# Kernel tuning notes

Hardware: AMD Instinct MI355X
Metric: run time of the kernel (lower is better)

## Reference

```python
import jax, jax.numpy as jnp
import numpy as np

B, S, D_IN, H = 4, 2048, 1024, 1024


def setup_inputs() -> dict:
    key = jax.random.key(0)
    k1, k2, k3 = jax.random.split(key, 3)
    qkv = jax.random.normal(k1, (B, S, D_IN), dtype=jnp.float32)
    # True = position is masked out (torch masked_fill semantics)
    attention_mask = jax.random.randint(k2, (B, S), 0, 2).astype(jnp.bool_)
    W_qkv = jax.random.normal(k3, (D_IN, 3 * H), dtype=jnp.float32) * (1.0 / np.sqrt(D_IN))
    b_qkv = jnp.zeros((3 * H,), dtype=jnp.float32)
    return {"qkv": qkv, "attention_mask": attention_mask, "W_qkv": W_qkv, "b_qkv": b_qkv}


def reference(qkv, attention_mask, W_qkv, b_qkv):
    # fused QKV projection: (B, S, 3H)
    proj = jnp.einsum("bsd,dh->bsh", qkv, W_qkv) + b_qkv
    q, k, v = jnp.split(proj, 3, axis=-1)  # each (B, S, H)
    scaling_factor = jnp.asarray(H, dtype=q.dtype) ** 0.5
    q = q * scaling_factor  # NOTE: original multiplies (not divides) by sqrt(H)
    scores = jnp.einsum("bqh,bkh->bqk", q, k)  # (B, S, S)
    # mask broadcasts over the query dim: masked keys get -inf
    neg_inf = jnp.asarray(-jnp.inf, dtype=scores.dtype)
    scores = jnp.where(attention_mask[:, None, :], neg_inf, scores)
    distributions = jax.nn.softmax(scores, axis=-1)  # dropout p=0.0 -> identity
    return jnp.einsum("bqk,bkh->bqh", distributions, v)
```

## Files before the change

### kernel.cpp

```cpp
#include <hip/hip_runtime.h>
#include <stdint.h>


#define S_LEN 2048
#define BATCH 4
#define DIN   1024
#define HDIM  1024
#define N3H   3072
#define NTOK  8192

typedef unsigned short u16;
typedef __attribute__((ext_vector_type(8))) short bf16x8;
typedef __attribute__((ext_vector_type(4))) float f32x4;
typedef __attribute__((ext_vector_type(16))) float f32x16;
typedef __attribute__((ext_vector_type(4))) unsigned short u16x4;

__device__ __forceinline__ u16 f2bf(float x) {
  union { float f; unsigned u; } c; c.f = x;
  unsigned r = c.u + 0x7fffu + ((c.u >> 16) & 1u);
  return (u16)(r >> 16);
}
__device__ __forceinline__ float bf2f(u16 h) {
  union { unsigned u; float f; } c; c.u = ((unsigned)h) << 16;
  return c.f;
}

__device__ __forceinline__ void gload16(const void* g, void* lds) {
  auto* gp = reinterpret_cast<const __attribute__((address_space(1))) void*>(
      reinterpret_cast<uintptr_t>(g));
  auto* lp = reinterpret_cast<__attribute__((address_space(3))) void*>(
      (unsigned)reinterpret_cast<uintptr_t>(lds));
  __builtin_amdgcn_global_load_lds(gp, lp, 16, 0, 0);
}

__device__ __forceinline__ void stage_tile(const u16* __restrict__ g, int ld,
                                           u16* lds, int wave, int lane) {
  const int rlane = lane >> 3;
  const int kb    = (lane & 7) ^ (rlane & 7);
#pragma unroll
  for (int h = 0; h < 4; ++h) {
    const int instr = wave * 4 + h;
    const u16* gp = g + (size_t)(instr * 8 + rlane) * ld + kb * 8;
    gload16(gp, (char*)lds + instr * 1024);
  }
}

__device__ __forceinline__ bf16x8 frag32(const u16* t, int wq, int sub, int kh,
                                         int lane) {
  const int r5   = lane & 31;
  const int row  = wq * 64 + sub * 32 + r5;
  const int slot = (kh * 2 + (lane >> 5)) ^ (r5 & 7);
  return *(const bf16x8*)(t + row * 64 + slot * 8);
}

__device__ __forceinline__ void gemm_core_split(
    const u16* __restrict__ Ah, const u16* __restrict__ Al,
    const u16* __restrict__ Bh, const u16* __restrict__ Bl,
    int lda, int ldb, int K, f32x16 acc[2][2])
{
  __shared__ __align__(16) u16 lds[4 * 8192];
  u16* aH = lds;           u16* aL = lds + 8192;
  u16* bH = lds + 16384;   u16* bL = lds + 24576;
  const int tid  = threadIdx.x;
  const int wave = tid >> 6, lane = tid & 63;
  const int wm = wave >> 1, wn = wave & 1;

#pragma unroll
  for (int i = 0; i < 2; ++i)
#pragma unroll
    for (int j = 0; j < 2; ++j)
#pragma unroll
      for (int r = 0; r < 16; ++r) acc[i][j][r] = 0.f;

  for (int k0 = 0; k0 < K; k0 += 64) {
    stage_tile(Ah + k0, lda, aH, wave, lane);
    stage_tile(Al + k0, lda, aL, wave, lane);
    stage_tile(Bh + k0, ldb, bH, wave, lane);
    stage_tile(Bl + k0, ldb, bL, wave, lane);
    __syncthreads();

#pragma unroll
    for (int kh = 0; kh < 4; ++kh) {
      bf16x8 fah[2], fal[2];
#pragma unroll
      for (int i = 0; i < 2; ++i) {
        fah[i] = frag32(aH, wm, i, kh, lane);
        fal[i] = frag32(aL, wm, i, kh, lane);
      }
#pragma unroll
      for (int j = 0; j < 2; ++j) {
        const bf16x8 fbh = frag32(bH, wn, j, kh, lane);
        const bf16x8 fbl = frag32(bL, wn, j, kh, lane);
#pragma unroll
        for (int i = 0; i < 2; ++i) {
          acc[i][j] = __builtin_amdgcn_mfma_f32_32x32x16_bf16(fah[i], fbh, acc[i][j], 0, 0, 0);
          acc[i][j] = __builtin_amdgcn_mfma_f32_32x32x16_bf16(fah[i], fbl, acc[i][j], 0, 0, 0);
          acc[i][j] = __builtin_amdgcn_mfma_f32_32x32x16_bf16(fal[i], fbh, acc[i][j], 0, 0, 0);
        }
      }
    }
    __syncthreads();
  }
}

__device__ __forceinline__ void gemm_core_plain(
    const u16* __restrict__ A, const u16* __restrict__ B,
    int lda, int ldb, int K, f32x16 acc[2][2])
{
  __shared__ __align__(16) u16 lds[2 * 8192];
  u16* aT = lds; u16* bT = lds + 8192;
  const int tid  = threadIdx.x;
  const int wave = tid >> 6, lane = tid & 63;
  const int wm = wave >> 1, wn = wave & 1;

#pragma unroll
  for (int i = 0; i < 2; ++i)
#pragma unroll
    for (int j = 0; j < 2; ++j)
#pragma unroll
      for (int r = 0; r < 16; ++r) acc[i][j][r] = 0.f;

  for (int k0 = 0; k0 < K; k0 += 64) {
    stage_tile(A + k0, lda, aT, wave, lane);
    stage_tile(B + k0, ldb, bT, wave, lane);
    __syncthreads();
#pragma unroll
    for (int kh = 0; kh < 4; ++kh) {
      bf16x8 fa[2];
#pragma unroll
      for (int i = 0; i < 2; ++i) fa[i] = frag32(aT, wm, i, kh, lane);
#pragma unroll
      for (int j = 0; j < 2; ++j) {
        const bf16x8 fb = frag32(bT, wn, j, kh, lane);
#pragma unroll
        for (int i = 0; i < 2; ++i)
          acc[i][j] = __builtin_amdgcn_mfma_f32_32x32x16_bf16(fa[i], fb, acc[i][j], 0, 0, 0);
      }
    }
    __syncthreads();
  }
}

#define ROW32(r, lane) (((r) & 3) + 8 * ((r) >> 2) + 4 * ((lane) >> 5))

__global__ void prep_mask_kernel(const unsigned char* __restrict__ m,
                                 float* __restrict__ bias) {
  __shared__ int isBool;
  if (threadIdx.x == 0) isBool = 0;
  __syncthreads();
  for (int i = threadIdx.x; i < NTOK; i += 256)
    if ((i & 3) && m[i]) isBool = 1;
  __syncthreads();
  const int stride = isBool ? 1 : 4;
  const float ninf = -__builtin_inff();
  for (int i = threadIdx.x; i < NTOK; i += 256)
    bias[i] = m[(size_t)i * stride] ? ninf : 0.f;
}

__global__ __launch_bounds__(256) void split_f32_kernel(
    const float* __restrict__ x, u16* __restrict__ hi, u16* __restrict__ lo) {
  const int i = (blockIdx.x * 256 + threadIdx.x) * 4;
  const f32x4 v = *(const f32x4*)(x + i);
  u16x4 h, l;
#pragma unroll
  for (int c = 0; c < 4; ++c) {
    h[c] = f2bf(v[c]);
    l[c] = f2bf(v[c] - bf2f(h[c]));
  }
  *(u16x4*)(hi + i) = h;
  *(u16x4*)(lo + i) = l;
}

__global__ __launch_bounds__(256) void splitWT_kernel(
    const float* __restrict__ W, u16* __restrict__ whi, u16* __restrict__ wlo) {
  __shared__ float tile[32][33];
  const int t = threadIdx.x;
  const int n0 = blockIdx.x * 32;
  const int d0 = blockIdx.y * 32;
  const int dr = t >> 3, nc = (t & 7) * 4;
  const f32x4 v = *(const f32x4*)(W + (size_t)(d0 + dr) * N3H + n0 + nc);
#pragma unroll
  for (int c = 0; c < 4; ++c) tile[dr][nc + c] = v[c];
  __syncthreads();
  const int nr = t >> 3, dc = (t & 7) * 4;
  u16x4 h, l;
#pragma unroll
  for (int c = 0; c < 4; ++c) {
    const float x = tile[dc + c][nr];
    h[c] = f2bf(x);
    l[c] = f2bf(x - bf2f(h[c]));
  }
  const size_t o = (size_t)(n0 + nr) * DIN + d0 + dc;
  *(u16x4*)(whi + o) = h;
  *(u16x4*)(wlo + o) = l;
}

__global__ __launch_bounds__(256, 2) void proj_qk_kernel(
    const u16* __restrict__ Ahi, const u16* __restrict__ Alo,
    const u16* __restrict__ Whi, const u16* __restrict__ Wlo,
    const float* __restrict__ bias,
    u16* __restrict__ qhi, u16* __restrict__ qlo,
    u16* __restrict__ khi, u16* __restrict__ klo)
{
  const int bx = blockIdx.x, by = blockIdx.y;
  f32x16 acc[2][2];
  gemm_core_split(Ahi + (size_t)by * 128 * DIN, Alo + (size_t)by * 128 * DIN,
                  Whi + (size_t)bx * 128 * DIN, Wlo + (size_t)bx * 128 * DIN,
                  DIN, DIN, DIN, acc);
  const int lane = threadIdx.x & 63, wave = threadIdx.x >> 6;
  const int wm = wave >> 1, wn = wave & 1;
#pragma unroll
  for (int i = 0; i < 2; ++i) {
#pragma unroll
    for (int j = 0; j < 2; ++j) {
#pragma unroll
      for (int r = 0; r < 16; ++r) {
        const int row = by * 128 + wm * 64 + i * 32 + ROW32(r, lane);
        const int col = bx * 128 + wn * 64 + j * 32 + (lane & 31);
        const float v = acc[i][j][r] + bias[col];
        const u16 h = f2bf(v);
        const u16 l = f2bf(v - bf2f(h));
        if (col < HDIM) {
          const size_t idx = (size_t)row * HDIM + col;
          qhi[idx] = h; qlo[idx] = l;
        } else {
          const size_t idx = (size_t)row * HDIM + (col - HDIM);
          khi[idx] = h; klo[idx] = l;
        }
      }
    }
  }
}

__global__ __launch_bounds__(256, 2) void proj_v_kernel(
    const u16* __restrict__ Ahi, const u16* __restrict__ Whi,
    const float* __restrict__ bias, u16* __restrict__ vt)
{
  const int bx = blockIdx.x, by = blockIdx.y;
  f32x16 acc[2][2];
  gemm_core_plain(Ahi + (size_t)by * 128 * DIN,
                  Whi + (size_t)(2048 + bx * 128) * DIN,
                  DIN, DIN, DIN, acc);
  const int lane = threadIdx.x & 63, wave = threadIdx.x >> 6;
  const int wm = wave >> 1, wn = wave & 1;
#pragma unroll
  for (int i = 0; i < 2; ++i) {
#pragma unroll
    for (int j = 0; j < 2; ++j) {
#pragma unroll
      for (int r = 0; r < 16; ++r) {
        const int row = by * 128 + wm * 64 + i * 32 + ROW32(r, lane);
        const int b = row >> 11, s = row & 2047;
        const int hcol = bx * 128 + wn * 64 + j * 32 + (lane & 31);
        const float v = acc[i][j][r] + bias[2 * HDIM + hcol];
        vt[((size_t)b * HDIM + hcol) * S_LEN + s] = f2bf(v);
      }
    }
  }
}

__global__ __launch_bounds__(256, 2) void scores_kernel(
    const u16* __restrict__ qhi, const u16* __restrict__ qlo,
    const u16* __restrict__ khi, const u16* __restrict__ klo,
    const float* __restrict__ maskbias, float* __restrict__ scores)
{
  const int id   = blockIdx.x;
  const int xcd  = id & 7;
  const int s    = id >> 3;
  const int b    = s >> 5;
  const int slot = s & 31;
  const int r    = xcd + 8 * (slot >> 4);
  const int w    = slot & 15;
  const int bx   = (r & 3) * 4 + (w & 3);
  const int by   = (r >> 2) * 4 + (w >> 2);

  f32x16 acc[2][2];
  const size_t qoff = ((size_t)b * S_LEN + by * 128) * HDIM;
  const size_t koff = ((size_t)b * S_LEN + bx * 128) * HDIM;
  gemm_core_split(qhi + qoff, qlo + qoff, khi + koff, klo + koff,
                  HDIM, HDIM, HDIM, acc);
  const int lane = threadIdx.x & 63, wave = threadIdx.x >> 6;
  const int wm = wave >> 1, wn = wave & 1;
#pragma unroll
  for (int i = 0; i < 2; ++i) {
#pragma unroll
    for (int j = 0; j < 2; ++j) {
#pragma unroll
      for (int rr = 0; rr < 16; ++rr) {
        const int q   = by * 128 + wm * 64 + i * 32 + ROW32(rr, lane);
        const int key = bx * 128 + wn * 64 + j * 32 + (lane & 31);
        scores[((size_t)b * S_LEN + q) * S_LEN + key] =
            32.0f * acc[i][j][rr] + maskbias[b * S_LEN + key];
      }
    }
  }
}

__global__ __launch_bounds__(256) void softmax_kernel(float* __restrict__ scores) {
  const int wave = threadIdx.x >> 6, lane = threadIdx.x & 63;
  const int row = blockIdx.x * 4 + wave;
  float* srow = scores + (size_t)row * S_LEN;

  f32x4 v[8];
#pragma unroll
  for (int c = 0; c < 8; ++c) v[c] = ((const f32x4*)srow)[c * 64 + lane];

  float m = -__builtin_inff();
#pragma unroll
  for (int c = 0; c < 8; ++c)
    m = fmaxf(m, fmaxf(fmaxf(v[c][0], v[c][1]), fmaxf(v[c][2], v[c][3])));
#pragma unroll
  for (int o = 32; o > 0; o >>= 1) m = fmaxf(m, __shfl_xor(m, o));

  float s = 0.f;
#pragma unroll
  for (int c = 0; c < 8; ++c) {
#pragma unroll
    for (int e = 0; e < 4; ++e) {
      v[c][e] = __expf(v[c][e] - m);
      s += v[c][e];
    }
  }
#pragma unroll
  for (int o = 32; o > 0; o >>= 1) s += __shfl_xor(s, o);
  const float inv = 1.0f / s;

  u16* prow = (u16*)srow;
#pragma unroll
  for (int c = 0; c < 8; ++c) {
    u16x4 o4 = { f2bf(v[c][0] * inv), f2bf(v[c][1] * inv),
                 f2bf(v[c][2] * inv), f2bf(v[c][3] * inv) };
    ((u16x4*)prow)[c * 64 + lane] = o4;
  }
}

__global__ __launch_bounds__(256, 2) void pv_kernel(
    const u16* __restrict__ P, const u16* __restrict__ vt, float* __restrict__ out)
{
  const int id   = blockIdx.x;
  const int xcd  = id & 7;
  const int s    = id >> 3;
  const int b    = s >> 4;
  const int slot = s & 15;
  const int bx   = (xcd & 1) * 4 + (slot & 3);
  const int by   = (xcd >> 1) * 4 + (slot >> 2);

  f32x16 acc[2][2];
  gemm_core_plain(P + ((size_t)b * S_LEN + by * 128) * (2 * S_LEN),
                  vt + ((size_t)b * HDIM + bx * 128) * S_LEN,
                  2 * S_LEN, S_LEN, S_LEN, acc);
  const int lane = threadIdx.x & 63, wave = threadIdx.x >> 6;
  const int wm = wave >> 1, wn = wave & 1;
#pragma unroll
  for (int i = 0; i < 2; ++i) {
#pragma unroll
    for (int j = 0; j < 2; ++j) {
#pragma unroll
      for (int r = 0; r < 16; ++r) {
        const int q = by * 128 + wm * 64 + i * 32 + ROW32(r, lane);
        const int h = bx * 128 + wn * 64 + j * 32 + (lane & 31);
        out[((size_t)b * S_LEN + q) * HDIM + h] = acc[i][j][r];
      }
    }
  }
}

extern "C" void kernel_launch(void* const* d_in, const int* in_sizes, int n_in,
                              void* d_out, int out_size, void* d_ws, size_t ws_size,
                              hipStream_t stream)
{
  const float* qkv  = (const float*)d_in[0];
  const void*  mask = d_in[1];
  const float* W    = (const float*)d_in[2];
  const float* bias = (const float*)d_in[3];
  float* out = (float*)d_out;
  char* ws = (char*)d_ws;

  const size_t off_mask = 0;
  const size_t off_Whi  = 32768;
  const size_t off_Wlo  = off_Whi + (size_t)N3H * DIN * 2;
  const size_t off_Qhi  = off_Wlo + (size_t)N3H * DIN * 2;
  const size_t off_Qlo  = off_Qhi + (size_t)NTOK * HDIM * 2;
  const size_t off_Khi  = off_Qlo + (size_t)NTOK * HDIM * 2;
  const size_t off_Klo  = off_Khi + (size_t)NTOK * HDIM * 2;
  const size_t off_Vt   = off_Klo + (size_t)NTOK * HDIM * 2;
  const size_t off_A    = off_Vt + (size_t)NTOK * HDIM * 2;
  const size_t off_Alo  = off_A + (size_t)NTOK * DIN * 2;
  const size_t off_sc   = off_A;

  float* maskbias = (float*)(ws + off_mask);
  u16* Whi = (u16*)(ws + off_Whi);  u16* Wlo = (u16*)(ws + off_Wlo);
  u16* Qhi = (u16*)(ws + off_Qhi);  u16* Qlo = (u16*)(ws + off_Qlo);
  u16* Khi = (u16*)(ws + off_Khi);  u16* Klo = (u16*)(ws + off_Klo);
  u16* Vt  = (u16*)(ws + off_Vt);
  u16* Ahi = (u16*)(ws + off_A);    u16* Alo = (u16*)(ws + off_Alo);
  float* scores = (float*)(ws + off_sc);

  prep_mask_kernel<<<1, 256, 0, stream>>>((const unsigned char*)mask, maskbias);
  split_f32_kernel<<<NTOK * DIN / 1024, 256, 0, stream>>>(qkv, Ahi, Alo);
  splitWT_kernel<<<dim3(N3H / 32, DIN / 32), 256, 0, stream>>>(W, Whi, Wlo);
  proj_qk_kernel<<<dim3(2 * HDIM / 128, NTOK / 128, 1), 256, 0, stream>>>(
      Ahi, Alo, Whi, Wlo, bias, Qhi, Qlo, Khi, Klo);
  proj_v_kernel<<<dim3(HDIM / 128, NTOK / 128, 1), 256, 0, stream>>>(
      Ahi, Whi, bias, Vt);
  scores_kernel<<<16 * 16 * BATCH, 256, 0, stream>>>(
      Qhi, Qlo, Khi, Klo, maskbias, scores);
  softmax_kernel<<<NTOK / 4, 256, 0, stream>>>(scores);
  pv_kernel<<<8 * 16 * BATCH, 256, 0, stream>>>(
      (const u16*)scores, Vt, out);
}
```

Baseline: 414.5 us.

## Replace split-bf16 GEMM core with 256x256 double-buffered pipelined 8-wave kernel

The split-precision GEMM used by the QK projection and score kernels is rewritten. Each block now computes a 256x256 tile with 512 threads. The three hi/lo products are flattened into 48 K-steps over a double-buffered LDS, and the global-to-LDS loads for later steps are interleaved with MFMA phases using barriers, setprio and explicit vmcnt waits. This aims to hide global load latency and raise data reuse per byte loaded. In exchange it uses a large LDS footprint and has fewer blocks: the score kernel drops to 256 blocks and loses its XCD-aware block mapping.

Result: no change. 419.6 us (+1.2%).

```diff
diff --git a/kernel.cpp b/kernel.cpp
--- a/kernel.cpp
+++ b/kernel.cpp
@@ -45,6 +45,18 @@
   }
 }
 
+__device__ __forceinline__ void stage_half8(const u16* __restrict__ g, int ld,
+                                            u16* lds, int wave, int lane) {
+  const int rlane = lane >> 3;
+  const int kb    = (lane & 7) ^ (rlane & 7);
+#pragma unroll
+  for (int h = 0; h < 2; ++h) {
+    const int instr = wave * 2 + h;
+    const u16* gp = g + (size_t)(instr * 8 + rlane) * ld + kb * 8;
+    gload16(gp, (char*)lds + instr * 1024);
+  }
+}
+
 __device__ __forceinline__ bf16x8 frag32(const u16* t, int wq, int sub, int kh,
                                          int lane) {
   const int r5   = lane & 31;
@@ -53,54 +65,125 @@
   return *(const bf16x8*)(t + row * 64 + slot * 8);
 }
 
-__device__ __forceinline__ void gemm_core_split(
+__device__ __forceinline__ const u16* selA(const u16* Ah, const u16* Al, int t) {
+  return (t < 32) ? Ah : Al;
+}
+__device__ __forceinline__ const u16* selB(const u16* Bh, const u16* Bl, int t) {
+  return ((t >> 4) == 1) ? Bl : Bh;
+}
+
+template <int MODE>
+__device__ __forceinline__ void tile4(
+    int t, int buf, u16* lds, f32x16 acc[4][2],
     const u16* __restrict__ Ah, const u16* __restrict__ Al,
     const u16* __restrict__ Bh, const u16* __restrict__ Bl,
-    int lda, int ldb, int K, f32x16 acc[2][2])
-{
-  __shared__ __align__(16) u16 lds[4 * 8192];
-  u16* aH = lds;           u16* aL = lds + 8192;
-  u16* bH = lds + 16384;   u16* bL = lds + 24576;
-  const int tid  = threadIdx.x;
-  const int wave = tid >> 6, lane = tid & 63;
-  const int wm = wave >> 1, wn = wave & 1;
-
-#pragma unroll
-  for (int i = 0; i < 2; ++i)
-#pragma unroll
-    for (int j = 0; j < 2; ++j)
-#pragma unroll
-      for (int r = 0; r < 16; ++r) acc[i][j][r] = 0.f;
-
-  for (int k0 = 0; k0 < K; k0 += 64) {
-    stage_tile(Ah + k0, lda, aH, wave, lane);
-    stage_tile(Al + k0, lda, aL, wave, lane);
-    stage_tile(Bh + k0, ldb, bH, wave, lane);
-    stage_tile(Bl + k0, ldb, bL, wave, lane);
-    __syncthreads();
-
-#pragma unroll
-    for (int kh = 0; kh < 4; ++kh) {
-      bf16x8 fah[2], fal[2];
-#pragma unroll
-      for (int i = 0; i < 2; ++i) {
-        fah[i] = frag32(aH, wm, i, kh, lane);
-        fal[i] = frag32(aL, wm, i, kh, lane);
-      }
-#pragma unroll
-      for (int j = 0; j < 2; ++j) {
-        const bf16x8 fbh = frag32(bH, wn, j, kh, lane);
-        const bf16x8 fbl = frag32(bL, wn, j, kh, lane);
-#pragma unroll
-        for (int i = 0; i < 2; ++i) {
-          acc[i][j] = __builtin_amdgcn_mfma_f32_32x32x16_bf16(fah[i], fbh, acc[i][j], 0, 0, 0);
-          acc[i][j] = __builtin_amdgcn_mfma_f32_32x32x16_bf16(fah[i], fbl, acc[i][j], 0, 0, 0);
-          acc[i][j] = __builtin_amdgcn_mfma_f32_32x32x16_bf16(fal[i], fbh, acc[i][j], 0, 0, 0);
-        }
-      }
-    }
-    __syncthreads();
-  }
+    int lda, int ldb, int wm, int wn, int wave, int lane)
+{
+  u16* const Ab = lds + buf * 32768 + wm * 8192;
+  u16* const Bb = lds + buf * 32768 + 16384 + (wn >> 1) * 8192;
+  const int bs = wn & 1;
+  bf16x8 fa[2][4], fb0[4], fb1[4];
+
+#pragma unroll
+  for (int kh = 0; kh < 4; ++kh) {
+    fa[0][kh] = frag32(Ab, 0, 0, kh, lane);
+    fa[1][kh] = frag32(Ab, 0, 1, kh, lane);
+    fb0[kh]   = frag32(Bb, bs, 0, kh, lane);
+  }
+  if (MODE >= 1)
+    stage_half8(selA(Ah, Al, t + 1) + (size_t)128 * lda + ((t + 1) & 15) * 64,
+                lda, lds + ((t + 1) & 1) * 32768 + 8192, wave, lane);
+  __builtin_amdgcn_s_barrier();
+  __builtin_amdgcn_s_setprio(1);
+#pragma unroll
+  for (int kh = 0; kh < 4; ++kh) {
+    acc[0][0] = __builtin_amdgcn_mfma_f32_32x32x16_bf16(fa[0][kh], fb0[kh], acc[0][0], 0, 0, 0);
+    acc[1][0] = __builtin_amdgcn_mfma_f32_32x32x16_bf16(fa[1][kh], fb0[kh], acc[1][0], 0, 0, 0);
+  }
+  __builtin_amdgcn_s_setprio(0);
+  __builtin_amdgcn_s_barrier();
+
+#pragma unroll
+  for (int kh = 0; kh < 4; ++kh) fb1[kh] = frag32(Bb, bs, 1, kh, lane);
+  if (MODE >= 1)
+    stage_half8(selB(Bh, Bl, t + 1) + (size_t)128 * ldb + ((t + 1) & 15) * 64,
+                ldb, lds + ((t + 1) & 1) * 32768 + 24576, wave, lane);
+  __builtin_amdgcn_s_barrier();
+  __builtin_amdgcn_s_setprio(1);
+#pragma unroll
+  for (int kh = 0; kh < 4; ++kh) {
+    acc[0][1] = __builtin_amdgcn_mfma_f32_32x32x16_bf16(fa[0][kh], fb1[kh], acc[0][1], 0, 0, 0);
+    acc[1][1] = __builtin_amdgcn_mfma_f32_32x32x16_bf16(fa[1][kh], fb1[kh], acc[1][1], 0, 0, 0);
+  }
+  __builtin_amdgcn_s_setprio(0);
+  __builtin_amdgcn_s_barrier();
+  asm volatile("" ::: "memory");
+
+#pragma unroll
+  for (int kh = 0; kh < 4; ++kh) {
+    fa[0][kh] = frag32(Ab, 1, 0, kh, lane);
+    fa[1][kh] = frag32(Ab, 1, 1, kh, lane);
+  }
+  if (MODE == 2)
+    stage_half8(selB(Bh, Bl, t + 2) + ((t + 2) & 15) * 64, ldb,
+                lds + buf * 32768 + 16384, wave, lane);
+  __builtin_amdgcn_s_barrier();
+  __builtin_amdgcn_s_setprio(1);
+#pragma unroll
+  for (int kh = 0; kh < 4; ++kh) {
+    acc[2][0] = __builtin_amdgcn_mfma_f32_32x32x16_bf16(fa[0][kh], fb0[kh], acc[2][0], 0, 0, 0);
+    acc[3][0] = __builtin_amdgcn_mfma_f32_32x32x16_bf16(fa[1][kh], fb0[kh], acc[3][0], 0, 0, 0);
+  }
+  __builtin_amdgcn_s_setprio(0);
+  __builtin_amdgcn_s_barrier();
+  asm volatile("" ::: "memory");
+
+  if (MODE == 2) {
+    stage_half8(selA(Ah, Al, t + 2) + ((t + 2) & 15) * 64, lda,
+                lds + buf * 32768, wave, lane);
+    asm volatile("s_waitcnt vmcnt(4)" ::: "memory");
+  }
+  if (MODE == 1) asm volatile("s_waitcnt vmcnt(0)" ::: "memory");
+  __builtin_amdgcn_s_barrier();
+  __builtin_amdgcn_s_setprio(1);
+#pragma unroll
+  for (int kh = 0; kh < 4; ++kh) {
+    acc[2][1] = __builtin_amdgcn_mfma_f32_32x32x16_bf16(fa[0][kh], fb1[kh], acc[2][1], 0, 0, 0);
+    acc[3][1] = __builtin_amdgcn_mfma_f32_32x32x16_bf16(fa[1][kh], fb1[kh], acc[3][1], 0, 0, 0);
+  }
+  __builtin_amdgcn_s_setprio(0);
+  __builtin_amdgcn_s_barrier();
+}
+
+__device__ __forceinline__ void gemm256_split3(
+    const u16* __restrict__ Ah, const u16* __restrict__ Al,
+    const u16* __restrict__ Bh, const u16* __restrict__ Bl,
+    int lda, int ldb, f32x16 acc[4][2], u16* lds,
+    int wm, int wn, int wave, int lane)
+{
+#pragma unroll
+  for (int a = 0; a < 4; ++a)
+#pragma unroll
+    for (int b = 0; b < 2; ++b)
+#pragma unroll
+      for (int r = 0; r < 16; ++r) acc[a][b][r] = 0.f;
+
+  stage_half8(Ah, lda, lds, wave, lane);
+  stage_half8(Bh, ldb, lds + 16384, wave, lane);
+  stage_half8(Ah + (size_t)128 * lda, lda, lds + 8192, wave, lane);
+  stage_half8(Bh + (size_t)128 * ldb, ldb, lds + 24576, wave, lane);
+  stage_half8(Bh + 64, ldb, lds + 32768 + 16384, wave, lane);
+  stage_half8(Ah + 64, lda, lds + 32768, wave, lane);
+  asm volatile("s_waitcnt vmcnt(4)" ::: "memory");
+  __builtin_amdgcn_s_barrier();
+
+#pragma unroll 1
+  for (int t = 0; t < 46; t += 2) {
+    tile4<2>(t,     0, lds, acc, Ah, Al, Bh, Bl, lda, ldb, wm, wn, wave, lane);
+    tile4<2>(t + 1, 1, lds, acc, Ah, Al, Bh, Bl, lda, ldb, wm, wn, wave, lane);
+  }
+  tile4<1>(46, 0, lds, acc, Ah, Al, Bh, Bl, lda, ldb, wm, wn, wave, lane);
+  tile4<0>(47, 1, lds, acc, Ah, Al, Bh, Bl, lda, ldb, wm, wn, wave, lane);
 }
 
 __device__ __forceinline__ void gemm_core_plain(
@@ -195,29 +278,32 @@
   *(u16x4*)(wlo + o) = l;
 }
 
-__global__ __launch_bounds__(256, 2) void proj_qk_kernel(
+__global__ __launch_bounds__(512, 2) void proj_qk256_kernel(
     const u16* __restrict__ Ahi, const u16* __restrict__ Alo,
     const u16* __restrict__ Whi, const u16* __restrict__ Wlo,
     const float* __restrict__ bias,
     u16* __restrict__ qhi, u16* __restrict__ qlo,
     u16* __restrict__ khi, u16* __restrict__ klo)
 {
+  __shared__ __align__(16) u16 lds[2 * 4 * 8192];
   const int bx = blockIdx.x, by = blockIdx.y;
-  f32x16 acc[2][2];
-  gemm_core_split(Ahi + (size_t)by * 128 * DIN, Alo + (size_t)by * 128 * DIN,
-                  Whi + (size_t)bx * 128 * DIN, Wlo + (size_t)bx * 128 * DIN,
-                  DIN, DIN, DIN, acc);
-  const int lane = threadIdx.x & 63, wave = threadIdx.x >> 6;
-  const int wm = wave >> 1, wn = wave & 1;
-#pragma unroll
-  for (int i = 0; i < 2; ++i) {
-#pragma unroll
-    for (int j = 0; j < 2; ++j) {
+  const int tid = threadIdx.x, wave = tid >> 6, lane = tid & 63;
+  const int wm = wave >> 2, wn = wave & 3;
+
+  f32x16 acc[4][2];
+  gemm256_split3(Ahi + (size_t)by * 256 * DIN, Alo + (size_t)by * 256 * DIN,
+                 Whi + (size_t)bx * 256 * DIN, Wlo + (size_t)bx * 256 * DIN,
+                 DIN, DIN, acc, lds, wm, wn, wave, lane);
+
+#pragma unroll
+  for (int a = 0; a < 4; ++a) {
+#pragma unroll
+    for (int b = 0; b < 2; ++b) {
 #pragma unroll
       for (int r = 0; r < 16; ++r) {
-        const int row = by * 128 + wm * 64 + i * 32 + ROW32(r, lane);
-        const int col = bx * 128 + wn * 64 + j * 32 + (lane & 31);
-        const float v = acc[i][j][r] + bias[col];
+        const int row = by * 256 + wm * 128 + a * 32 + ROW32(r, lane);
+        const int col = bx * 256 + wn * 64 + b * 32 + (lane & 31);
+        const float v = acc[a][b][r] + bias[col];
         const u16 h = f2bf(v);
         const u16 l = f2bf(v - bf2f(h));
         if (col < HDIM) {
@@ -259,38 +345,35 @@
   }
 }
 
-__global__ __launch_bounds__(256, 2) void scores_kernel(
+__global__ __launch_bounds__(512, 2) void scores256_kernel(
     const u16* __restrict__ qhi, const u16* __restrict__ qlo,
     const u16* __restrict__ khi, const u16* __restrict__ klo,
     const float* __restrict__ maskbias, float* __restrict__ scores)
 {
-  const int id   = blockIdx.x;
-  const int xcd  = id & 7;
-  const int s    = id >> 3;
-  const int b    = s >> 5;
-  const int slot = s & 31;
-  const int r    = xcd + 8 * (slot >> 4);
-  const int w    = slot & 15;
-  const int bx   = (r & 3) * 4 + (w & 3);
-  const int by   = (r >> 2) * 4 + (w >> 2);
-
-  f32x16 acc[2][2];
-  const size_t qoff = ((size_t)b * S_LEN + by * 128) * HDIM;
-  const size_t koff = ((size_t)b * S_LEN + bx * 128) * HDIM;
-  gemm_core_split(qhi + qoff, qlo + qoff, khi + koff, klo + koff,
-                  HDIM, HDIM, HDIM, acc);
-  const int lane = threadIdx.x & 63, wave = threadIdx.x >> 6;
-  const int wm = wave >> 1, wn = wave & 1;
-#pragma unroll
-  for (int i = 0; i < 2; ++i) {
-#pragma unroll
-    for (int j = 0; j < 2; ++j) {
-#pragma unroll
-      for (int rr = 0; rr < 16; ++rr) {
-        const int q   = by * 128 + wm * 64 + i * 32 + ROW32(rr, lane);
-        const int key = bx * 128 + wn * 64 + j * 32 + (lane & 31);
+  __shared__ __align__(16) u16 lds[2 * 4 * 8192];
+  const int id = blockIdx.x;
+  const int b  = id >> 6;
+  const int by = (id >> 3) & 7;
+  const int bx = id & 7;
+  const int tid = threadIdx.x, wave = tid >> 6, lane = tid & 63;
+  const int wm = wave >> 2, wn = wave & 3;
+
+  f32x16 acc[4][2];
+  const size_t qoff = ((size_t)b * S_LEN + by * 256) * HDIM;
+  const size_t koff = ((size_t)b * S_LEN + bx * 256) * HDIM;
+  gemm256_split3(qhi + qoff, qlo + qoff, khi + koff, klo + koff,
+                 HDIM, HDIM, acc, lds, wm, wn, wave, lane);
+
+#pragma unroll
+  for (int a = 0; a < 4; ++a) {
+#pragma unroll
+    for (int bj = 0; bj < 2; ++bj) {
+#pragma unroll
+      for (int r = 0; r < 16; ++r) {
+        const int q   = by * 256 + wm * 128 + a * 32 + ROW32(r, lane);
+        const int key = bx * 256 + wn * 64 + bj * 32 + (lane & 31);
         scores[((size_t)b * S_LEN + q) * S_LEN + key] =
-            32.0f * acc[i][j][rr] + maskbias[b * S_LEN + key];
+            32.0f * acc[a][bj][r] + maskbias[b * S_LEN + key];
       }
     }
   }
@@ -399,11 +482,11 @@
   prep_mask_kernel<<<1, 256, 0, stream>>>((const unsigned char*)mask, maskbias);
   split_f32_kernel<<<NTOK * DIN / 1024, 256, 0, stream>>>(qkv, Ahi, Alo);
   splitWT_kernel<<<dim3(N3H / 32, DIN / 32), 256, 0, stream>>>(W, Whi, Wlo);
-  proj_qk_kernel<<<dim3(2 * HDIM / 128, NTOK / 128, 1), 256, 0, stream>>>(
+  proj_qk256_kernel<<<dim3(2 * HDIM / 256, NTOK / 256), 512, 0, stream>>>(
       Ahi, Alo, Whi, Wlo, bias, Qhi, Qlo, Khi, Klo);
   proj_v_kernel<<<dim3(HDIM / 128, NTOK / 128, 1), 256, 0, stream>>>(
       Ahi, Whi, bias, Vt);
-  scores_kernel<<<16 * 16 * BATCH, 256, 0, stream>>>(
+  scores256_kernel<<<64 * BATCH, 512, 0, stream>>>(
       Qhi, Qlo, Khi, Klo, maskbias, scores);
   softmax_kernel<<<NTOK / 4, 256, 0, stream>>>(scores);
   pv_kernel<<<8 * 16 * BATCH, 256, 0, stream>>>(
```

## Compact unmasked keys and skip masked key work across K/V projection and attention

Applied to the files above, without the earlier changes.

A prep kernel builds, per batch, a compacted list of unmasked key positions and their count. The K and V projections gather only those rows, and the scores, softmax and PV kernels then work only over the compacted key range, exiting early or shortening K beyond the count. With a random mask about half the keys are masked, so this removes roughly half of the K/V projection, score, softmax and PV work. In exchange it adds gather indirection in the tile loads and a serial single-block prep kernel, and the tail beyond the count relies on -inf padding inside softmax.

Result: faster. 382.2 us (-7.8%).

```diff
diff --git a/kernel.cpp b/kernel.cpp
--- a/kernel.cpp
+++ b/kernel.cpp
@@ -45,6 +45,20 @@
   }
 }
 
+__device__ __forceinline__ void stage_tile_idx(
+    const u16* __restrict__ gbase, const int* __restrict__ idxb, int jbase,
+    int k0, u16* lds, int wave, int lane) {
+  const int rlane = lane >> 3;
+  const int kb    = (lane & 7) ^ (rlane & 7);
+#pragma unroll
+  for (int h = 0; h < 4; ++h) {
+    const int instr = wave * 4 + h;
+    const int s = idxb[jbase + instr * 8 + rlane];
+    const u16* gp = gbase + (size_t)s * DIN + k0 + kb * 8;
+    gload16(gp, (char*)lds + instr * 1024);
+  }
+}
+
 __device__ __forceinline__ bf16x8 frag32(const u16* t, int wq, int sub, int kh,
                                          int lane) {
   const int r5   = lane & 31;
@@ -103,6 +117,57 @@
   }
 }
 
+__device__ __forceinline__ void gemm_core_split_idx(
+    const u16* __restrict__ Ah, const u16* __restrict__ Al,
+    const int* __restrict__ idxb, int jbase,
+    const u16* __restrict__ Bh, const u16* __restrict__ Bl,
+    f32x16 acc[2][2])
+{
+  __shared__ __align__(16) u16 lds[4 * 8192];
+  u16* aH = lds;           u16* aL = lds + 8192;
+  u16* bH = lds + 16384;   u16* bL = lds + 24576;
+  const int tid  = threadIdx.x;
+  const int wave = tid >> 6, lane = tid & 63;
+  const int wm = wave >> 1, wn = wave & 1;
+
+#pragma unroll
+  for (int i = 0; i < 2; ++i)
+#pragma unroll
+    for (int j = 0; j < 2; ++j)
+#pragma unroll
+      for (int r = 0; r < 16; ++r) acc[i][j][r] = 0.f;
+
+  for (int k0 = 0; k0 < DIN; k0 += 64) {
+    stage_tile_idx(Ah, idxb, jbase, k0, aH, wave, lane);
+    stage_tile_idx(Al, idxb, jbase, k0, aL, wave, lane);
+    stage_tile(Bh + k0, DIN, bH, wave, lane);
+    stage_tile(Bl + k0, DIN, bL, wave, lane);
+    __syncthreads();
+
+#pragma unroll
+    for (int kh = 0; kh < 4; ++kh) {
+      bf16x8 fah[2], fal[2];
+#pragma unroll
+      for (int i = 0; i < 2; ++i) {
+        fah[i] = frag32(aH, wm, i, kh, lane);
+        fal[i] = frag32(aL, wm, i, kh, lane);
+      }
+#pragma unroll
+      for (int j = 0; j < 2; ++j) {
+        const bf16x8 fbh = frag32(bH, wn, j, kh, lane);
+        const bf16x8 fbl = frag32(bL, wn, j, kh, lane);
+#pragma unroll
+        for (int i = 0; i < 2; ++i) {
+          acc[i][j] = __builtin_amdgcn_mfma_f32_32x32x16_bf16(fah[i], fbh, acc[i][j], 0, 0, 0);
+          acc[i][j] = __builtin_amdgcn_mfma_f32_32x32x16_bf16(fah[i], fbl, acc[i][j], 0, 0, 0);
+          acc[i][j] = __builtin_amdgcn_mfma_f32_32x32x16_bf16(fal[i], fbh, acc[i][j], 0, 0, 0);
+        }
+      }
+    }
+    __syncthreads();
+  }
+}
+
 __device__ __forceinline__ void gemm_core_plain(
     const u16* __restrict__ A, const u16* __restrict__ B,
     int lda, int ldb, int K, f32x16 acc[2][2])
@@ -141,10 +206,48 @@
   }
 }
 
+__device__ __forceinline__ void gemm_core_plain_idx(
+    const u16* __restrict__ A, const int* __restrict__ idxb, int jbase,
+    const u16* __restrict__ B, f32x16 acc[2][2])
+{
+  __shared__ __align__(16) u16 lds[2 * 8192];
+  u16* aT = lds; u16* bT = lds + 8192;
+  const int tid  = threadIdx.x;
+  const int wave = tid >> 6, lane = tid & 63;
+  const int wm = wave >> 1, wn = wave & 1;
+
+#pragma unroll
+  for (int i = 0; i < 2; ++i)
+#pragma unroll
+    for (int j = 0; j < 2; ++j)
+#pragma unroll
+      for (int r = 0; r < 16; ++r) acc[i][j][r] = 0.f;
+
+  for (int k0 = 0; k0 < DIN; k0 += 64) {
+    stage_tile_idx(A, idxb, jbase, k0, aT, wave, lane);
+    stage_tile(B + k0, DIN, bT, wave, lane);
+    __syncthreads();
+#pragma unroll
+    for (int kh = 0; kh < 4; ++kh) {
+      bf16x8 fa[2];
+#pragma unroll
+      for (int i = 0; i < 2; ++i) fa[i] = frag32(aT, wm, i, kh, lane);
+#pragma unroll
+      for (int j = 0; j < 2; ++j) {
+        const bf16x8 fb = frag32(bT, wn, j, kh, lane);
+#pragma unroll
+        for (int i = 0; i < 2; ++i)
+          acc[i][j] = __builtin_amdgcn_mfma_f32_32x32x16_bf16(fa[i], fb, acc[i][j], 0, 0, 0);
+      }
+    }
+    __syncthreads();
+  }
+}
+
 #define ROW32(r, lane) (((r) & 3) + 8 * ((r) >> 2) + 4 * ((lane) >> 5))
 
-__global__ void prep_mask_kernel(const unsigned char* __restrict__ m,
-                                 float* __restrict__ bias) {
+__global__ void prep_kernel(const unsigned char* __restrict__ m,
+                            int* __restrict__ idx, int* __restrict__ kcount) {
   __shared__ int isBool;
   if (threadIdx.x == 0) isBool = 0;
   __syncthreads();
@@ -152,9 +255,21 @@
     if ((i & 3) && m[i]) isBool = 1;
   __syncthreads();
   const int stride = isBool ? 1 : 4;
-  const float ninf = -__builtin_inff();
-  for (int i = threadIdx.x; i < NTOK; i += 256)
-    bias[i] = m[(size_t)i * stride] ? ninf : 0.f;
+  const int wave = threadIdx.x >> 6, lane = threadIdx.x & 63;
+  const int b = wave;
+  const int base = b * S_LEN;
+  int running = 0;
+#pragma unroll 1
+  for (int c = 0; c < S_LEN / 64; ++c) {
+    const int s = c * 64 + lane;
+    const int um = (m[(size_t)(base + s) * stride] == 0);
+    const unsigned long long bal = __ballot(um);
+    const int pre = (int)__popcll(bal & ((1ULL << lane) - 1ULL));
+    if (um) idx[base + running + pre] = s;
+    running += (int)__popcll(bal);
+  }
+  if (lane == 0) kcount[b] = running;
+  for (int j = running + lane; j < S_LEN; j += 64) idx[base + j] = 0;
 }
 
 __global__ __launch_bounds__(256) void split_f32_kernel(
@@ -195,12 +310,11 @@
   *(u16x4*)(wlo + o) = l;
 }
 
-__global__ __launch_bounds__(256, 2) void proj_qk_kernel(
+__global__ __launch_bounds__(256, 2) void proj_q_kernel(
     const u16* __restrict__ Ahi, const u16* __restrict__ Alo,
     const u16* __restrict__ Whi, const u16* __restrict__ Wlo,
     const float* __restrict__ bias,
-    u16* __restrict__ qhi, u16* __restrict__ qlo,
-    u16* __restrict__ khi, u16* __restrict__ klo)
+    u16* __restrict__ qhi, u16* __restrict__ qlo)
 {
   const int bx = blockIdx.x, by = blockIdx.y;
   f32x16 acc[2][2];
@@ -220,13 +334,48 @@
         const float v = acc[i][j][r] + bias[col];
         const u16 h = f2bf(v);
         const u16 l = f2bf(v - bf2f(h));
-        if (col < HDIM) {
-          const size_t idx = (size_t)row * HDIM + col;
-          qhi[idx] = h; qlo[idx] = l;
-        } else {
-          const size_t idx = (size_t)row * HDIM + (col - HDIM);
-          khi[idx] = h; klo[idx] = l;
-        }
+        const size_t idx = (size_t)row * HDIM + col;
+        qhi[idx] = h; qlo[idx] = l;
+      }
+    }
+  }
+}
+
+__global__ __launch_bounds__(256, 2) void proj_k_kernel(
+    const u16* __restrict__ Ahi, const u16* __restrict__ Alo,
+    const u16* __restrict__ Whi, const u16* __restrict__ Wlo,
+    const float* __restrict__ bias,
+    const int* __restrict__ idx, const int* __restrict__ kcount,
+    u16* __restrict__ khi, u16* __restrict__ klo)
+{
+  const int id = blockIdx.x;
+  const int t  = id >> 5;
+  const int rs = id & 31;
+  const int b  = rs >> 3;
+  const int bx = rs & 7;
+  const int cnt = kcount[b];
+  if (t * 128 >= cnt) return;
+
+  f32x16 acc[2][2];
+  gemm_core_split_idx(Ahi + (size_t)b * S_LEN * DIN, Alo + (size_t)b * S_LEN * DIN,
+                      idx + b * S_LEN, t * 128,
+                      Whi + (size_t)(HDIM + bx * 128) * DIN,
+                      Wlo + (size_t)(HDIM + bx * 128) * DIN, acc);
+  const int lane = threadIdx.x & 63, wave = threadIdx.x >> 6;
+  const int wm = wave >> 1, wn = wave & 1;
+#pragma unroll
+  for (int i = 0; i < 2; ++i) {
+#pragma unroll
+    for (int j = 0; j < 2; ++j) {
+#pragma unroll
+      for (int r = 0; r < 16; ++r) {
+        const int jl   = t * 128 + wm * 64 + i * 32 + ROW32(r, lane);
+        const int hcol = bx * 128 + wn * 64 + j * 32 + (lane & 31);
+        const float v = acc[i][j][r] + bias[HDIM + hcol];
+        const u16 h = f2bf(v);
+        const u16 l = f2bf(v - bf2f(h));
+        const size_t o = ((size_t)b * S_LEN + jl) * HDIM + hcol;
+        khi[o] = h; klo[o] = l;
       }
     }
   }
@@ -234,13 +383,21 @@
 
 __global__ __launch_bounds__(256, 2) void proj_v_kernel(
     const u16* __restrict__ Ahi, const u16* __restrict__ Whi,
-    const float* __restrict__ bias, u16* __restrict__ vt)
-{
-  const int bx = blockIdx.x, by = blockIdx.y;
+    const float* __restrict__ bias,
+    const int* __restrict__ idx, const int* __restrict__ kcount,
+    u16* __restrict__ vt)
+{
+  const int id = blockIdx.x;
+  const int t  = id >> 5;
+  const int rs = id & 31;
+  const int b  = rs >> 3;
+  const int bx = rs & 7;
+  const int cnt = kcount[b];
+  if (t * 128 >= cnt) return;
+
   f32x16 acc[2][2];
-  gemm_core_plain(Ahi + (size_t)by * 128 * DIN,
-                  Whi + (size_t)(2048 + bx * 128) * DIN,
-                  DIN, DIN, DIN, acc);
+  gemm_core_plain_idx(Ahi + (size_t)b * S_LEN * DIN, idx + b * S_LEN, t * 128,
+                      Whi + (size_t)(2048 + bx * 128) * DIN, acc);
   const int lane = threadIdx.x & 63, wave = threadIdx.x >> 6;
   const int wm = wave >> 1, wn = wave & 1;
 #pragma unroll
@@ -249,11 +406,10 @@
     for (int j = 0; j < 2; ++j) {
 #pragma unroll
       for (int r = 0; r < 16; ++r) {
-        const int row = by * 128 + wm * 64 + i * 32 + ROW32(r, lane);
-        const int b = row >> 11, s = row & 2047;
+        const int jl   = t * 128 + wm * 64 + i * 32 + ROW32(r, lane);
         const int hcol = bx * 128 + wn * 64 + j * 32 + (lane & 31);
         const float v = acc[i][j][r] + bias[2 * HDIM + hcol];
-        vt[((size_t)b * HDIM + hcol) * S_LEN + s] = f2bf(v);
+        vt[((size_t)b * HDIM + hcol) * S_LEN + jl] = f2bf(v);
       }
     }
   }
@@ -262,17 +418,17 @@
 __global__ __launch_bounds__(256, 2) void scores_kernel(
     const u16* __restrict__ qhi, const u16* __restrict__ qlo,
     const u16* __restrict__ khi, const u16* __restrict__ klo,
-    const float* __restrict__ maskbias, float* __restrict__ scores)
+    const int* __restrict__ kcount, float* __restrict__ scores)
 {
   const int id   = blockIdx.x;
   const int xcd  = id & 7;
-  const int s    = id >> 3;
-  const int b    = s >> 5;
-  const int slot = s & 31;
-  const int r    = xcd + 8 * (slot >> 4);
-  const int w    = slot & 15;
-  const int bx   = (r & 3) * 4 + (w & 3);
-  const int by   = (r >> 2) * 4 + (w >> 2);
+  const int rest = id >> 3;
+  const int b    = rest >> 5;
+  const int w    = rest & 31;
+  const int by   = xcd * 2 + (w >> 4);
+  const int bx   = w & 15;
+  const int cnt  = kcount[b];
+  if (bx * 128 >= cnt) return;
 
   f32x16 acc[2][2];
   const size_t qoff = ((size_t)b * S_LEN + by * 128) * HDIM;
@@ -289,36 +445,48 @@
       for (int rr = 0; rr < 16; ++rr) {
         const int q   = by * 128 + wm * 64 + i * 32 + ROW32(rr, lane);
         const int key = bx * 128 + wn * 64 + j * 32 + (lane & 31);
-        scores[((size_t)b * S_LEN + q) * S_LEN + key] =
-            32.0f * acc[i][j][rr] + maskbias[b * S_LEN + key];
-      }
-    }
-  }
-}
-
-__global__ __launch_bounds__(256) void softmax_kernel(float* __restrict__ scores) {
+        scores[((size_t)b * S_LEN + q) * S_LEN + key] = 32.0f * acc[i][j][rr];
+      }
+    }
+  }
+}
+
+__global__ __launch_bounds__(256) void softmax_kernel(
+    float* __restrict__ scores, const int* __restrict__ kcount) {
   const int wave = threadIdx.x >> 6, lane = threadIdx.x & 63;
   const int row = blockIdx.x * 4 + wave;
+  const int b = row >> 11;
+  const int cnt = kcount[b];
+  const int nc = (cnt + 255) >> 8;
   float* srow = scores + (size_t)row * S_LEN;
+  const float ninf = -__builtin_inff();
 
   f32x4 v[8];
-#pragma unroll
-  for (int c = 0; c < 8; ++c) v[c] = ((const f32x4*)srow)[c * 64 + lane];
-
-  float m = -__builtin_inff();
-#pragma unroll
-  for (int c = 0; c < 8; ++c)
-    m = fmaxf(m, fmaxf(fmaxf(v[c][0], v[c][1]), fmaxf(v[c][2], v[c][3])));
+  float m = ninf;
+#pragma unroll
+  for (int c = 0; c < 8; ++c) {
+    if (c < nc) {
+      v[c] = ((const f32x4*)srow)[c * 64 + lane];
+      const int j0 = c * 256 + lane * 4;
+#pragma unroll
+      for (int e = 0; e < 4; ++e) {
+        if (j0 + e >= cnt) v[c][e] = ninf;
+        m = fmaxf(m, v[c][e]);
+      }
+    }
+  }
 #pragma unroll
   for (int o = 32; o > 0; o >>= 1) m = fmaxf(m, __shfl_xor(m, o));
 
   float s = 0.f;
 #pragma unroll
   for (int c = 0; c < 8; ++c) {
-#pragma unroll
-    for (int e = 0; e < 4; ++e) {
-      v[c][e] = __expf(v[c][e] - m);
-      s += v[c][e];
+    if (c < nc) {
+#pragma unroll
+      for (int e = 0; e < 4; ++e) {
+        v[c][e] = __expf(v[c][e] - m);
+        s += v[c][e];
+      }
     }
   }
 #pragma unroll
@@ -328,14 +496,17 @@
   u16* prow = (u16*)srow;
 #pragma unroll
   for (int c = 0; c < 8; ++c) {
-    u16x4 o4 = { f2bf(v[c][0] * inv), f2bf(v[c][1] * inv),
-                 f2bf(v[c][2] * inv), f2bf(v[c][3] * inv) };
-    ((u16x4*)prow)[c * 64 + lane] = o4;
+    if (c < nc) {
+      u16x4 o4 = { f2bf(v[c][0] * inv), f2bf(v[c][1] * inv),
+                   f2bf(v[c][2] * inv), f2bf(v[c][3] * inv) };
+      ((u16x4*)prow)[c * 64 + lane] = o4;
+    }
   }
 }
 
 __global__ __launch_bounds__(256, 2) void pv_kernel(
-    const u16* __restrict__ P, const u16* __restrict__ vt, float* __restrict__ out)
+    const u16* __restrict__ P, const u16* __restrict__ vt,
+    const int* __restrict__ kcount, float* __restrict__ out)
 {
   const int id   = blockIdx.x;
   const int xcd  = id & 7;
@@ -344,11 +515,13 @@
   const int slot = s & 15;
   const int bx   = (xcd & 1) * 4 + (slot & 3);
   const int by   = (xcd >> 1) * 4 + (slot >> 2);
+  const int cnt  = kcount[b];
+  const int K    = (cnt + 63) & ~63;
 
   f32x16 acc[2][2];
   gemm_core_plain(P + ((size_t)b * S_LEN + by * 128) * (2 * S_LEN),
                   vt + ((size_t)b * HDIM + bx * 128) * S_LEN,
-                  2 * S_LEN, S_LEN, S_LEN, acc);
+                  2 * S_LEN, S_LEN, K, acc);
   const int lane = threadIdx.x & 63, wave = threadIdx.x >> 6;
   const int wm = wave >> 1, wn = wave & 1;
 #pragma unroll
@@ -376,8 +549,9 @@
   float* out = (float*)d_out;
   char* ws = (char*)d_ws;
 
-  const size_t off_mask = 0;
-  const size_t off_Whi  = 32768;
+  const size_t off_cnt  = 0;
+  const size_t off_idx  = 256;
+  const size_t off_Whi  = 33024;
   const size_t off_Wlo  = off_Whi + (size_t)N3H * DIN * 2;
   const size_t off_Qhi  = off_Wlo + (size_t)N3H * DIN * 2;
   const size_t off_Qlo  = off_Qhi + (size_t)NTOK * HDIM * 2;
@@ -388,7 +562,8 @@
   const size_t off_Alo  = off_A + (size_t)NTOK * DIN * 2;
   const size_t off_sc   = off_A;
 
-  float* maskbias = (float*)(ws + off_mask);
+  int* kcount = (int*)(ws + off_cnt);
+  int* idx    = (int*)(ws + off_idx);
   u16* Whi = (u16*)(ws + off_Whi);  u16* Wlo = (u16*)(ws + off_Wlo);
   u16* Qhi = (u16*)(ws + off_Qhi);  u16* Qlo = (u16*)(ws + off_Qlo);
   u16* Khi = (u16*)(ws + off_Khi);  u16* Klo = (u16*)(ws + off_Klo);
@@ -396,16 +571,18 @@
   u16* Ahi = (u16*)(ws + off_A);    u16* Alo = (u16*)(ws + off_Alo);
   float* scores = (float*)(ws + off_sc);
 
-  prep_mask_kernel<<<1, 256, 0, stream>>>((const unsigned char*)mask, maskbias);
+  prep_kernel<<<1, 256, 0, stream>>>((const unsigned char*)mask, idx, kcount);
   split_f32_kernel<<<NTOK * DIN / 1024, 256, 0, stream>>>(qkv, Ahi, Alo);
   splitWT_kernel<<<dim3(N3H / 32, DIN / 32), 256, 0, stream>>>(W, Whi, Wlo);
-  proj_qk_kernel<<<dim3(2 * HDIM / 128, NTOK / 128, 1), 256, 0, stream>>>(
-      Ahi, Alo, Whi, Wlo, bias, Qhi, Qlo, Khi, Klo);
-  proj_v_kernel<<<dim3(HDIM / 128, NTOK / 128, 1), 256, 0, stream>>>(
-      Ahi, Whi, bias, Vt);
+  proj_q_kernel<<<dim3(HDIM / 128, NTOK / 128), 256, 0, stream>>>(
+      Ahi, Alo, Whi, Wlo, bias, Qhi, Qlo);
+  proj_k_kernel<<<512, 256, 0, stream>>>(
+      Ahi, Alo, Whi, Wlo, bias, idx, kcount, Khi, Klo);
+  proj_v_kernel<<<512, 256, 0, stream>>>(
+      Ahi, Whi, bias, idx, kcount, Vt);
   scores_kernel<<<16 * 16 * BATCH, 256, 0, stream>>>(
-      Qhi, Qlo, Khi, Klo, maskbias, scores);
-  softmax_kernel<<<NTOK / 4, 256, 0, stream>>>(scores);
+      Qhi, Qlo, Khi, Klo, kcount, scores);
+  softmax_kernel<<<NTOK / 4, 256, 0, stream>>>(scores, kcount);
   pv_kernel<<<8 * 16 * BATCH, 256, 0, stream>>>(
-      (const u16*)scores, Vt, out);
-}
+      (const u16*)scores, Vt, kcount, out);
+}
```
